# Optimization experiments

Hardware: AMD Instinct MI355X
Metric: run time of the kernel (lower is better)

The kernel has to match this reference:

```python
import jax, jax.numpy as jnp
import numpy as np

TOL = 1e-5
CLIP_MAX = 1e5


def _mlp(z, W1, b1, W2, b2, W3, b3):
    # small per-edge MLP: 76 -> 32 -> 32 -> 1, scalar output per edge
    h1 = jax.nn.relu(z @ W1 + b1)
    h2 = jax.nn.relu(h1 @ W2 + b2)
    return (h2 @ W3 + b3)[..., 0]


def setup_inputs() -> dict:
    key = jax.random.key(0)
    ks = jax.random.split(key, 8)
    B, N, DH, DX, DE = 8, 256, 32, 3, 4
    D_IN = 2 * (DX + DH + 1) + DE  # 76
    h = jax.random.normal(ks[0], (B, N, DH), dtype=jnp.float32)
    e = jax.random.uniform(ks[1], (B, N, N, DE), dtype=jnp.float32)
    x = jax.random.normal(ks[2], (B, N, DX), dtype=jnp.float32)
    q = jax.random.normal(ks[3], (B, N, 1), dtype=jnp.float32)
    mask = jnp.ones((B, N, N, 1), dtype=jnp.float32)
    W1 = jax.random.normal(ks[4], (D_IN, 32), dtype=jnp.float32) * (1.0 / np.sqrt(D_IN))
    b1 = jnp.zeros((32,), dtype=jnp.float32)
    W2 = jax.random.normal(ks[5], (32, 32), dtype=jnp.float32) * (1.0 / np.sqrt(32))
    b2 = jnp.zeros((32,), dtype=jnp.float32)
    W3 = jax.random.normal(ks[6], (32, 1), dtype=jnp.float32) * (1.0 / np.sqrt(32))
    b3 = jnp.zeros((1,), dtype=jnp.float32)
    return {"h": h, "e": e, "x": x, "q": q, "mask": mask,
            "W1": W1, "b1": b1, "W2": W2, "b2": b2, "W3": W3, "b3": b3}


def reference(h, e, x, q, mask, W1, b1, W2, b2, W3, b3):
    T = 1
    B, N = e.shape[0], e.shape[1]
    clip = jnp.clip(e, TOL, CLIP_MAX)
    largest_e = jnp.max(clip, axis=-1)                      # [B,N,N]
    is_near = (largest_e != TOL).astype(jnp.float32)        # [B,N,N]
    mask_red = jnp.max(mask, axis=-1)                       # [B,N,N]
    for _ in range(T):
        inp_atom = jnp.concatenate([x, h, q], axis=-1)      # [B,N,D]
        D = inp_atom.shape[-1]
        inp_i = jnp.broadcast_to(inp_atom[:, :, None, :], (B, N, N, D))
        inp_j = jnp.transpose(inp_i, (0, 2, 1, 3))
        inp_ij = jnp.concatenate([inp_i, inp_j, e], axis=-1)  # [B,N,N,2D+De]
        inp_ji = jnp.concatenate([inp_j, inp_i, e], axis=-1)
        elec_ij = _mlp(inp_ij, W1, b1, W2, b2, W3, b3)      # [B,N,N]
        elec_ji = _mlp(inp_ji, W1, b1, W2, b2, W3, b3)
        antisym = 0.5 * (elec_ij - elec_ji) * mask_red * is_near
        q = q + jnp.sum(antisym, axis=2)[..., None]          # [B,N,1]
    return q
```

## Files before the change

kernel.cpp:

```cpp
#include <hip/hip_runtime.h>
#include <hip/hip_bf16.h>

#define TOL_F 1e-5f
#define CLIP_MAX_F 1e5f

typedef __attribute__((ext_vector_type(8))) short v8s;
typedef __attribute__((ext_vector_type(4))) float v4f;

__device__ inline unsigned short f2bf(float f) {
    __hip_bfloat16 t = __float2bfloat16(f);
    union { __hip_bfloat16 b; unsigned short u; } cv;
    cv.b = t;
    return cv.u;
}

__global__ __launch_bounds__(256) void precompute_kernel(
    const float* __restrict__ h,
    const float* __restrict__ x,
    const float* __restrict__ q,
    const float* __restrict__ W1,
    float* __restrict__ AT)
{
    const int gid = blockIdx.x * 256 + threadIdx.x;
    const int n  = gid >> 6;
    const int cc = gid & 63;
    const int c  = cc & 31;
    const int rowbase = (cc < 32) ? 0 : 36;
    const float* Wcol = W1 + rowbase * 32 + c;

    const float* xp = x + n * 3;
    float acc = xp[0] * Wcol[0];
    acc = fmaf(xp[1], Wcol[32], acc);
    acc = fmaf(xp[2], Wcol[64], acc);
    const float* hp = h + n * 32;
    #pragma unroll
    for (int k = 0; k < 32; ++k)
        acc = fmaf(hp[k], Wcol[(3 + k) * 32], acc);
    acc = fmaf(q[n], Wcol[35 * 32], acc);

    AT[n * 64 + cc] = acc;
}

__global__ __launch_bounds__(256) void edge_kernel(
    const float* __restrict__ e,
    const float* __restrict__ q,
    const float* __restrict__ mask,
    const float* __restrict__ W1,
    const float* __restrict__ b1,
    const float* __restrict__ W2,
    const float* __restrict__ b2,
    const float* __restrict__ W3,
    const float* __restrict__ AT,
    float* __restrict__ out)
{
    const int b = blockIdx.x >> 8;
    const int i = blockIdx.x & 255;
    const int lane = threadIdx.x & 63;
    const int wv = threadIdx.x >> 6;
    const int oc = lane & 15;
    const int kg = lane >> 4;
    const int c0 = kg * 8;

    v8s B0, B1;
    {
        union { unsigned short u[8]; v8s v; } ub0, ub1;
        #pragma unroll
        for (int jj = 0; jj < 8; ++jj) {
            ub0.u[jj] = f2bf(W2[(c0 + jj) * 32 + oc]);
            ub1.u[jj] = f2bf(W2[(c0 + jj) * 32 + oc + 16]);
        }
        B0 = ub0.v; B1 = ub1.v;
    }
    const float b2a = b2[oc], b2b = b2[oc + 16];
    const float w3a = W3[oc], w3b = W3[oc + 16];

    const float* ATi = AT + (b * 256 + i) * 64;
    float base_a[8], base_b[8];
    float We[4][8];
    #pragma unroll
    for (int jj = 0; jj < 8; ++jj) {
        const float bb = b1[c0 + jj];
        base_a[jj] = ATi[c0 + jj] + bb;
        base_b[jj] = ATi[32 + c0 + jj] + bb;
        #pragma unroll
        for (int t = 0; t < 4; ++t)
            We[t][jj] = W1[(72 + t) * 32 + c0 + jj];
    }

    const v4f Z = {0.f, 0.f, 0.f, 0.f};
    float qacc = 0.f;

    #pragma unroll
    for (int t = 0; t < 4; ++t) {
        const int jE = wv * 64 + t * 16 + oc;
        const int eoff = (b * 256 + i) * 256 + jE;

        const float4 ev = ((const float4*)e)[eoff];
        const float m = mask[eoff];
        const float cl0 = fminf(fmaxf(ev.x, TOL_F), CLIP_MAX_F);
        const float cl1 = fminf(fmaxf(ev.y, TOL_F), CLIP_MAX_F);
        const float cl2 = fminf(fmaxf(ev.z, TOL_F), CLIP_MAX_F);
        const float cl3 = fminf(fmaxf(ev.w, TOL_F), CLIP_MAX_F);
        const float largest = fmaxf(fmaxf(cl0, cl1), fmaxf(cl2, cl3));
        const float nearf = (largest != TOL_F) ? 1.0f : 0.0f;
        const float scale = 0.5f * m * nearf;

        const float4* ATj4 = (const float4*)(AT + (b * 256 + jE) * 64);
        const float4 lo0 = ATj4[kg * 2],     lo1 = ATj4[kg * 2 + 1];
        const float4 hi0 = ATj4[8 + kg * 2], hi1 = ATj4[9 + kg * 2];
        const float alo[8] = {lo0.x, lo0.y, lo0.z, lo0.w, lo1.x, lo1.y, lo1.z, lo1.w};
        const float ahi[8] = {hi0.x, hi0.y, hi0.z, hi0.w, hi1.x, hi1.y, hi1.z, hi1.w};

        union { unsigned short u[8]; v8s v; } ua, ub;
        #pragma unroll
        for (int jj = 0; jj < 8; ++jj) {
            float ew = We[0][jj] * ev.x;
            ew = fmaf(We[1][jj], ev.y, ew);
            ew = fmaf(We[2][jj], ev.z, ew);
            ew = fmaf(We[3][jj], ev.w, ew);
            const float pa = base_a[jj] + ahi[jj] + ew;
            const float pb = base_b[jj] + alo[jj] + ew;
            ua.u[jj] = f2bf(fmaxf(pa, 0.f));
            ub.u[jj] = f2bf(fmaxf(pb, 0.f));
        }

        v4f Da0 = __builtin_amdgcn_mfma_f32_16x16x32_bf16(ua.v, B0, Z, 0, 0, 0);
        v4f Da1 = __builtin_amdgcn_mfma_f32_16x16x32_bf16(ua.v, B1, Z, 0, 0, 0);
        v4f Db0 = __builtin_amdgcn_mfma_f32_16x16x32_bf16(ub.v, B0, Z, 0, 0, 0);
        v4f Db1 = __builtin_amdgcn_mfma_f32_16x16x32_bf16(ub.v, B1, Z, 0, 0, 0);

        #pragma unroll
        for (int r = 0; r < 4; ++r) {
            float va = fmaxf(Da1[r] + b2b, 0.f) * w3b;
            va = fmaf(fmaxf(Da0[r] + b2a, 0.f), w3a, va);
            float vb = fmaxf(Db1[r] + b2b, 0.f) * w3b;
            vb = fmaf(fmaxf(Db0[r] + b2a, 0.f), w3a, vb);
            const float sc = __shfl(scale, kg * 4 + r, 64);
            qacc += (va - vb) * sc;
        }
    }

    #pragma unroll
    for (int off = 32; off > 0; off >>= 1)
        qacc += __shfl_down(qacc, off, 64);
    __shared__ float sRed[4];
    if (lane == 0) sRed[wv] = qacc;
    __syncthreads();
    if (threadIdx.x == 0) {
        out[b * 256 + i] = q[b * 256 + i] + (sRed[0] + sRed[1] + sRed[2] + sRed[3]);
    }
}

extern "C" void kernel_launch(void* const* d_in, const int* in_sizes, int n_in,
                              void* d_out, int out_size, void* d_ws, size_t ws_size,
                              hipStream_t stream) {
    const float* h    = (const float*)d_in[0];
    const float* e    = (const float*)d_in[1];
    const float* x    = (const float*)d_in[2];
    const float* q    = (const float*)d_in[3];
    const float* mask = (const float*)d_in[4];
    const float* W1   = (const float*)d_in[5];
    const float* b1   = (const float*)d_in[6];
    const float* W2   = (const float*)d_in[7];
    const float* b2   = (const float*)d_in[8];
    const float* W3   = (const float*)d_in[9];
    float* out = (float*)d_out;
    float* AT  = (float*)d_ws;

    hipLaunchKernelGGL(precompute_kernel, dim3(512), dim3(256), 0, stream,
                       h, x, q, W1, AT);
    hipLaunchKernelGGL(edge_kernel, dim3(8 * 256), dim3(256), 0, stream,
                       e, q, mask, W1, b1, W2, b2, W3, AT, out);
}
```

Baseline: 103.6 us.

## Process two source atoms per block and defer W3 projection to end

Each block now handles two consecutive i rows instead of one, halving the grid and reusing the per-j AT loads, the W2 bf16 fragments and the W1 edge weights across both rows. The W3 multiply and the 0.5 factor are hoisted out of the inner loop. Per-lane accumulators are kept per output half and combined with W3 only once at the end, which cuts per-edge arithmetic. This raises register pressure and halves the block count to 1024, which may reduce occupancy or latency hiding.

```diff
diff --git a/kernel.cpp b/kernel.cpp
--- a/kernel.cpp
+++ b/kernel.cpp
@@ -53,8 +53,9 @@
     const float* __restrict__ AT,
     float* __restrict__ out)
 {
-    const int b = blockIdx.x >> 8;
-    const int i = blockIdx.x & 255;
+    const int b  = blockIdx.x >> 7;
+    const int i0 = (blockIdx.x & 127) * 2;
+    const int i1 = i0 + 1;
     const int lane = threadIdx.x & 63;
     const int wv = threadIdx.x >> 6;
     const int oc = lane & 15;
@@ -72,82 +73,106 @@
         B0 = ub0.v; B1 = ub1.v;
     }
     const float b2a = b2[oc], b2b = b2[oc + 16];
-    const float w3a = W3[oc], w3b = W3[oc + 16];
 
-    const float* ATi = AT + (b * 256 + i) * 64;
-    float base_a[8], base_b[8];
+    const float* ATi0 = AT + (b * 256 + i0) * 64;
+    const float* ATi1 = AT + (b * 256 + i1) * 64;
+    float ba0[8], bb0[8], ba1[8], bb1[8];
     float We[4][8];
     #pragma unroll
     for (int jj = 0; jj < 8; ++jj) {
         const float bb = b1[c0 + jj];
-        base_a[jj] = ATi[c0 + jj] + bb;
-        base_b[jj] = ATi[32 + c0 + jj] + bb;
+        ba0[jj] = ATi0[c0 + jj] + bb;
+        bb0[jj] = ATi0[32 + c0 + jj] + bb;
+        ba1[jj] = ATi1[c0 + jj] + bb;
+        bb1[jj] = ATi1[32 + c0 + jj] + bb;
         #pragma unroll
         for (int t = 0; t < 4; ++t)
             We[t][jj] = W1[(72 + t) * 32 + c0 + jj];
     }
 
     const v4f Z = {0.f, 0.f, 0.f, 0.f};
-    float qacc = 0.f;
+    float accA0 = 0.f, accB0 = 0.f, accA1 = 0.f, accB1 = 0.f;
 
     #pragma unroll
     for (int t = 0; t < 4; ++t) {
         const int jE = wv * 64 + t * 16 + oc;
-        const int eoff = (b * 256 + i) * 256 + jE;
+        const int eoff = (b * 256 + i0) * 256 + jE;
 
-        const float4 ev = ((const float4*)e)[eoff];
-        const float m = mask[eoff];
-        const float cl0 = fminf(fmaxf(ev.x, TOL_F), CLIP_MAX_F);
-        const float cl1 = fminf(fmaxf(ev.y, TOL_F), CLIP_MAX_F);
-        const float cl2 = fminf(fmaxf(ev.z, TOL_F), CLIP_MAX_F);
-        const float cl3 = fminf(fmaxf(ev.w, TOL_F), CLIP_MAX_F);
-        const float largest = fmaxf(fmaxf(cl0, cl1), fmaxf(cl2, cl3));
-        const float nearf = (largest != TOL_F) ? 1.0f : 0.0f;
-        const float scale = 0.5f * m * nearf;
-
+        const float4 ev0 = ((const float4*)e)[eoff];
+        const float4 ev1 = ((const float4*)e)[eoff + 256];
+        const float m0 = mask[eoff];
+        const float m1 = mask[eoff + 256];
         const float4* ATj4 = (const float4*)(AT + (b * 256 + jE) * 64);
         const float4 lo0 = ATj4[kg * 2],     lo1 = ATj4[kg * 2 + 1];
         const float4 hi0 = ATj4[8 + kg * 2], hi1 = ATj4[9 + kg * 2];
         const float alo[8] = {lo0.x, lo0.y, lo0.z, lo0.w, lo1.x, lo1.y, lo1.z, lo1.w};
         const float ahi[8] = {hi0.x, hi0.y, hi0.z, hi0.w, hi1.x, hi1.y, hi1.z, hi1.w};
 
-        union { unsigned short u[8]; v8s v; } ua, ub;
+        float cl0 = fminf(fmaxf(ev0.x, TOL_F), CLIP_MAX_F);
+        float cl1 = fminf(fmaxf(ev0.y, TOL_F), CLIP_MAX_F);
+        float cl2 = fminf(fmaxf(ev0.z, TOL_F), CLIP_MAX_F);
+        float cl3 = fminf(fmaxf(ev0.w, TOL_F), CLIP_MAX_F);
+        float lg0 = fmaxf(fmaxf(cl0, cl1), fmaxf(cl2, cl3));
+        const float scale0 = (lg0 != TOL_F) ? m0 : 0.0f;
+        cl0 = fminf(fmaxf(ev1.x, TOL_F), CLIP_MAX_F);
+        cl1 = fminf(fmaxf(ev1.y, TOL_F), CLIP_MAX_F);
+        cl2 = fminf(fmaxf(ev1.z, TOL_F), CLIP_MAX_F);
+        cl3 = fminf(fmaxf(ev1.w, TOL_F), CLIP_MAX_F);
+        float lg1 = fmaxf(fmaxf(cl0, cl1), fmaxf(cl2, cl3));
+        const float scale1 = (lg1 != TOL_F) ? m1 : 0.0f;
+
+        union { unsigned short u[8]; v8s v; } ua0, ub0v, ua1, ub1v;
         #pragma unroll
         for (int jj = 0; jj < 8; ++jj) {
-            float ew = We[0][jj] * ev.x;
-            ew = fmaf(We[1][jj], ev.y, ew);
-            ew = fmaf(We[2][jj], ev.z, ew);
-            ew = fmaf(We[3][jj], ev.w, ew);
-            const float pa = base_a[jj] + ahi[jj] + ew;
-            const float pb = base_b[jj] + alo[jj] + ew;
-            ua.u[jj] = f2bf(fmaxf(pa, 0.f));
-            ub.u[jj] = f2bf(fmaxf(pb, 0.f));
+            float ew0 = We[0][jj] * ev0.x;
+            ew0 = fmaf(We[1][jj], ev0.y, ew0);
+            ew0 = fmaf(We[2][jj], ev0.z, ew0);
+            ew0 = fmaf(We[3][jj], ev0.w, ew0);
+            float ew1 = We[0][jj] * ev1.x;
+            ew1 = fmaf(We[1][jj], ev1.y, ew1);
+            ew1 = fmaf(We[2][jj], ev1.z, ew1);
+            ew1 = fmaf(We[3][jj], ev1.w, ew1);
+            ua0.u[jj]  = f2bf(fmaxf(ba0[jj] + ahi[jj] + ew0, 0.f));
+            ub0v.u[jj] = f2bf(fmaxf(bb0[jj] + alo[jj] + ew0, 0.f));
+            ua1.u[jj]  = f2bf(fmaxf(ba1[jj] + ahi[jj] + ew1, 0.f));
+            ub1v.u[jj] = f2bf(fmaxf(bb1[jj] + alo[jj] + ew1, 0.f));
         }
 
-        v4f Da0 = __builtin_amdgcn_mfma_f32_16x16x32_bf16(ua.v, B0, Z, 0, 0, 0);
-        v4f Da1 = __builtin_amdgcn_mfma_f32_16x16x32_bf16(ua.v, B1, Z, 0, 0, 0);
-        v4f Db0 = __builtin_amdgcn_mfma_f32_16x16x32_bf16(ub.v, B0, Z, 0, 0, 0);
-        v4f Db1 = __builtin_amdgcn_mfma_f32_16x16x32_bf16(ub.v, B1, Z, 0, 0, 0);
+        v4f Da00 = __builtin_amdgcn_mfma_f32_16x16x32_bf16(ua0.v,  B0, Z, 0, 0, 0);
+        v4f Da01 = __builtin_amdgcn_mfma_f32_16x16x32_bf16(ua0.v,  B1, Z, 0, 0, 0);
+        v4f Db00 = __builtin_amdgcn_mfma_f32_16x16x32_bf16(ub0v.v, B0, Z, 0, 0, 0);
+        v4f Db01 = __builtin_amdgcn_mfma_f32_16x16x32_bf16(ub0v.v, B1, Z, 0, 0, 0);
+        v4f Da10 = __builtin_amdgcn_mfma_f32_16x16x32_bf16(ua1.v,  B0, Z, 0, 0, 0);
+        v4f Da11 = __builtin_amdgcn_mfma_f32_16x16x32_bf16(ua1.v,  B1, Z, 0, 0, 0);
+        v4f Db10 = __builtin_amdgcn_mfma_f32_16x16x32_bf16(ub1v.v, B0, Z, 0, 0, 0);
+        v4f Db11 = __builtin_amdgcn_mfma_f32_16x16x32_bf16(ub1v.v, B1, Z, 0, 0, 0);
 
         #pragma unroll
         for (int r = 0; r < 4; ++r) {
-            float va = fmaxf(Da1[r] + b2b, 0.f) * w3b;
-            va = fmaf(fmaxf(Da0[r] + b2a, 0.f), w3a, va);
-            float vb = fmaxf(Db1[r] + b2b, 0.f) * w3b;
-            vb = fmaf(fmaxf(Db0[r] + b2a, 0.f), w3a, vb);
-            const float sc = __shfl(scale, kg * 4 + r, 64);
-            qacc += (va - vb) * sc;
+            const float sc0 = __shfl(scale0, kg * 4 + r, 64);
+            const float sc1 = __shfl(scale1, kg * 4 + r, 64);
+            accA0 += sc0 * (fmaxf(Da00[r] + b2a, 0.f) - fmaxf(Db00[r] + b2a, 0.f));
+            accB0 += sc0 * (fmaxf(Da01[r] + b2b, 0.f) - fmaxf(Db01[r] + b2b, 0.f));
+            accA1 += sc1 * (fmaxf(Da10[r] + b2a, 0.f) - fmaxf(Db10[r] + b2a, 0.f));
+            accB1 += sc1 * (fmaxf(Da11[r] + b2b, 0.f) - fmaxf(Db11[r] + b2b, 0.f));
         }
     }
 
+    const float w3a = W3[oc], w3b = W3[oc + 16];
+    float v0 = 0.5f * (accA0 * w3a + accB0 * w3b);
+    float v1 = 0.5f * (accA1 * w3a + accB1 * w3b);
+
     #pragma unroll
-    for (int off = 32; off > 0; off >>= 1)
-        qacc += __shfl_down(qacc, off, 64);
-    __shared__ float sRed[4];
-    if (lane == 0) sRed[wv] = qacc;
+    for (int off = 32; off > 0; off >>= 1) {
+        v0 += __shfl_down(v0, off, 64);
+        v1 += __shfl_down(v1, off, 64);
+    }
+    __shared__ float sRed[2][4];
+    if (lane == 0) { sRed[0][wv] = v0; sRed[1][wv] = v1; }
     __syncthreads();
     if (threadIdx.x == 0) {
-        out[b * 256 + i] = q[b * 256 + i] + (sRed[0] + sRed[1] + sRed[2] + sRed[3]);
+        out[b * 256 + i0] = q[b * 256 + i0] + (sRed[0][0] + sRed[0][1] + sRed[0][2] + sRed[0][3]);
+        out[b * 256 + i1] = q[b * 256 + i1] + (sRed[1][0] + sRed[1][1] + sRed[1][2] + sRed[1][3]);
     }
 }
 
@@ -169,6 +194,6 @@
 
     hipLaunchKernelGGL(precompute_kernel, dim3(512), dim3(256), 0, stream,
                        h, x, q, W1, AT);
-    hipLaunchKernelGGL(edge_kernel, dim3(8 * 256), dim3(256), 0, stream,
+    hipLaunchKernelGGL(edge_kernel, dim3(8 * 128), dim3(256), 0, stream,
                        e, q, mask, W1, b1, W2, b2, W3, AT, out);
 }
```

Measured after the change: 97.62 us. 1.06x faster.
